# Kernel optimization log

Hardware: AMD Instinct MI355X
Metric: run time of the kernel (lower is better)

The kernel has to match this reference:

```python
import jax, jax.numpy as jnp
import numpy as np

D = 128          # lattice edge (Z = Y = X = 128)
S = 8            # state_size
H = 16           # hidden_size
IN = 7 * S       # own state + 6 neighbor states = 56


def setup_inputs() -> dict:
    key = jax.random.key(0)
    k0, k1, k2 = jax.random.split(key, 3)
    N = D * D * D
    states = jax.random.normal(k0, (N, S), dtype=jnp.float32)
    W1 = jax.random.normal(k1, (IN, H), dtype=jnp.float32) * (1.0 / np.sqrt(IN))
    b1 = jnp.zeros((H,), dtype=jnp.float32)
    W2 = jax.random.normal(k2, (H, S), dtype=jnp.float32) * (1.0 / np.sqrt(H))
    b2 = jnp.zeros((S,), dtype=jnp.float32)
    return {"states": states, "W1": W1, "b1": b1, "W2": W2, "b2": b2}


def reference(states, W1, b1, W2, b2):
    # linear index = z*(X*Y) + y*X + x  ->  grid layout (Z, Y, X, S)
    g = states.reshape(D, D, D, S)
    # 6-neighbor gather with periodic boundary (NEIGHBOR_DIRECTIONS order:
    # (-1,0,0),(1,0,0),(0,-1,0),(0,1,0),(0,0,-1),(0,0,1)); x->axis2, y->axis1, z->axis0.
    # roll(+1) along an axis fetches the neighbor in the -1 direction.
    nbrs = [
        jnp.roll(g,  1, axis=2),  # x-1
        jnp.roll(g, -1, axis=2),  # x+1
        jnp.roll(g,  1, axis=1),  # y-1
        jnp.roll(g, -1, axis=1),  # y+1
        jnp.roll(g,  1, axis=0),  # z-1
        jnp.roll(g, -1, axis=0),  # z+1
    ]
    inp = jnp.concatenate([g] + nbrs, axis=-1)          # (Z, Y, X, 56)
    h = jnp.tanh(jnp.einsum('zyxi,ih->zyxh', inp, W1) + b1)
    out = jnp.einsum('zyxh,hs->zyxs', h, W2) + b2        # (Z, Y, X, 8)
    return out.reshape(-1, S)
```

## Files before the change

kernel.cpp:

```cpp
#include <hip/hip_runtime.h>

#define DIM 128
#define SLOT_STRIDE 2096

typedef __attribute__((ext_vector_type(8))) short bf16x8;
typedef __attribute__((ext_vector_type(4))) float f32x4;
typedef __attribute__((ext_vector_type(4))) unsigned int u32x4;

static __device__ __forceinline__ unsigned short f2bf_rne(float f) {
    union { float f; unsigned int i; } c; c.f = f;
    unsigned int u = c.i;
    return (unsigned short)((u + 0x7fffu + ((u >> 16) & 1u)) >> 16);
}
static __device__ __forceinline__ unsigned int fbits(float f) {
    union { float f; unsigned int i; } c; c.f = f; return c.i;
}
static __device__ __forceinline__ unsigned int pack_bf16_rne(float lo, float hi) {
    unsigned int ul = fbits(lo), uh = fbits(hi);
    unsigned int tl = ul + 0x7fffu + ((ul >> 16) & 1u);
    unsigned int th = uh + 0x7fffu + ((uh >> 16) & 1u);
    return __builtin_amdgcn_perm(th, tl, 0x07060302u);
}

struct Frags {
    bf16x8 w1h0, w1h1, w2h;
    f32x4 b1v, b2v;
};

static __device__ __forceinline__ void build_frags(
    const float* W1, const float* b1, const float* W2, const float* b2,
    int col, int quad, Frags& F)
{
#pragma unroll
    for (int j = 0; j < 8; ++j) {
        int k0 = quad * 8 + j;
        F.w1h0[j] = (short)f2bf_rne(W1[k0 * 16 + col]);
        int k1 = 32 + quad * 8 + j;
        F.w1h1[j] = (short)f2bf_rne((k1 < 56) ? W1[k1 * 16 + col] : 0.0f);
        float w2 = (j < 4 && col < 8) ? W2[(quad * 4 + j) * 8 + col] : 0.0f;
        F.w2h[j] = (short)f2bf_rne(w2);
    }
#pragma unroll
    for (int r = 0; r < 4; ++r) {
        F.b1v[r] = b1[quad * 4 + r];
        F.b2v[r] = (quad < 2) ? b2[quad * 4 + r] : 0.0f;
    }
}

__global__ __launch_bounds__(64) void setup_kernel(
    const float* __restrict__ W1, const float* __restrict__ b1,
    const float* __restrict__ W2, const float* __restrict__ b2,
    u32x4* __restrict__ ws)
{
    const int lane = threadIdx.x;
    Frags F;
    build_frags(W1, b1, W2, b2, lane & 15, lane >> 4, F);
    union { bf16x8 v; u32x4 u; } c;
    c.v = F.w1h0; ws[0 * 64 + lane] = c.u;
    c.v = F.w1h1; ws[1 * 64 + lane] = c.u;
    c.v = F.w2h;  ws[2 * 64 + lane] = c.u;
    union { f32x4 v; u32x4 u; } b;
    b.v = F.b1v; ws[3 * 64 + lane] = b.u;
    b.v = F.b2v; ws[4 * 64 + lane] = b.u;
}

template<bool USE_WS>
__global__ __launch_bounds__(256, 5) void lattice_kernel(
    const float* __restrict__ states,
    const float* __restrict__ W1, const float* __restrict__ b1,
    const float* __restrict__ W2, const float* __restrict__ b2,
    float* __restrict__ out, const u32x4* __restrict__ ws)
{
    __shared__ __align__(16) unsigned char lds[15 * SLOT_STRIDE];

    const int tid  = threadIdx.x;
    const int lane = tid & 63;
    const int w    = __builtin_amdgcn_readfirstlane(tid >> 6);
    const int col  = lane & 15;
    const int quad = lane >> 4;

    Frags F;
    if (USE_WS) {
        union { u32x4 u; bf16x8 v; } c;
        c.u = ws[0 * 64 + lane]; F.w1h0 = c.v;
        c.u = ws[1 * 64 + lane]; F.w1h1 = c.v;
        c.u = ws[2 * 64 + lane]; F.w2h  = c.v;
        union { u32x4 u; f32x4 v; } b;
        b.u = ws[3 * 64 + lane]; F.b1v = b.v;
        b.u = ws[4 * 64 + lane]; F.b2v = b.v;
    } else {
        build_frags(W1, b1, W2, b2, col, quad, F);
    }

    const int bI   = blockIdx.x;
    const int slab = bI & 7;
    const int inr  = bI >> 3;
    const int z    = slab * 16 + (inr >> 5);
    const int y0   = (inr & 31) << 2;

    f32x4 ga[7], gb[7];
#pragma unroll
    for (int i = 0; i < 7; ++i) {
        const int tk   = w * 7 + i;
        const int slot = (tk < 20) ? (tk >> 1) : 11 + ((tk - 20) >> 1);
        const int half = tk & 1;
        int yr, zr;
        if (slot < 6)       { yr = (y0 - 1 + slot) & 127; zr = z; }
        else if (slot < 10) { yr = y0 + (slot - 6);       zr = (z - 1) & 127; }
        else                { yr = y0 + (slot - 11);      zr = (z + 1) & 127; }
        const float* g = states + ((size_t)(zr * 16384 + yr * 128 + half * 64) << 3);
        ga[i] = *(const f32x4*)(g + (lane << 3));
        gb[i] = *(const f32x4*)(g + (lane << 3) + 4);
    }
#pragma unroll
    for (int i = 0; i < 7; ++i) {
        const int tk   = w * 7 + i;
        const int slot = (tk < 20) ? (tk >> 1) : 11 + ((tk - 20) >> 1);
        const int half = tk & 1;
        u32x4 p;
        p[0] = __builtin_amdgcn_perm(fbits(ga[i][1]), fbits(ga[i][0]), 0x07060302u);
        p[1] = __builtin_amdgcn_perm(fbits(ga[i][3]), fbits(ga[i][2]), 0x07060302u);
        p[2] = __builtin_amdgcn_perm(fbits(gb[i][1]), fbits(gb[i][0]), 0x07060302u);
        p[3] = __builtin_amdgcn_perm(fbits(gb[i][3]), fbits(gb[i][2]), 0x07060302u);
        const int base = slot * SLOT_STRIDE;
        *(u32x4*)(lds + base + ((half * 64 + lane + 1) << 4)) = p;
        if (half == 0 && lane == 0)  *(u32x4*)(lds + base + 2064) = p;
        if (half == 1 && lane == 63) *(u32x4*)(lds + base) = p;
    }
    __syncthreads();

    const int dxA   = (quad == 1) ? -1 : (quad == 2) ? 1 : 0;
    const int slotA = (quad == 3) ? w : w + 1;
    const int slotB = (quad == 1) ? 6 + w : (quad == 2) ? 11 + w : w + 2;
    const unsigned char* pA = lds + slotA * SLOT_STRIDE + ((col + dxA + 1) << 4);
    const unsigned char* pB = lds + slotB * SLOT_STRIDE + ((col + 1) << 4);

    float* pO = out + (size_t)((z * 16384 + (y0 + w) * 128 + col) * 8 + quad * 4);

#pragma unroll
    for (int i = 0; i < 8; ++i) {
        bf16x8 s0f = *(const bf16x8*)(pA + (i << 8));
        bf16x8 s1f = *(const bf16x8*)(pB + (i << 8));

        f32x4 acc = F.b1v;
        acc = __builtin_amdgcn_mfma_f32_16x16x32_bf16(F.w1h0, s0f, acc, 0, 0, 0);
        acc = __builtin_amdgcn_mfma_f32_16x16x32_bf16(F.w1h1, s1f, acc, 0, 0, 0);

        float h0t, h1t, h2t, h3t;
        {
            float e;
            e = __expf(2.0f * acc[0]); h0t = 1.0f - 2.0f * __builtin_amdgcn_rcpf(e + 1.0f);
            e = __expf(2.0f * acc[1]); h1t = 1.0f - 2.0f * __builtin_amdgcn_rcpf(e + 1.0f);
            e = __expf(2.0f * acc[2]); h2t = 1.0f - 2.0f * __builtin_amdgcn_rcpf(e + 1.0f);
            e = __expf(2.0f * acc[3]); h3t = 1.0f - 2.0f * __builtin_amdgcn_rcpf(e + 1.0f);
        }
        union { bf16x8 v; unsigned int u[4]; } hf;
        hf.u[0] = pack_bf16_rne(h0t, h1t);
        hf.u[1] = pack_bf16_rne(h2t, h3t);
        hf.u[2] = 0u;
        hf.u[3] = 0u;

        f32x4 acc2 = F.b2v;
        acc2 = __builtin_amdgcn_mfma_f32_16x16x32_bf16(F.w2h, hf.v, acc2, 0, 0, 0);

        if (quad < 2) {
            __builtin_nontemporal_store(acc2, (f32x4*)(pO + (i << 7)));
        }
    }
}

extern "C" void kernel_launch(void* const* d_in, const int* in_sizes, int n_in,
                              void* d_out, int out_size, void* d_ws, size_t ws_size,
                              hipStream_t stream) {
    const float* states = (const float*)d_in[0];
    const float* W1     = (const float*)d_in[1];
    const float* b1     = (const float*)d_in[2];
    const float* W2     = (const float*)d_in[3];
    const float* b2     = (const float*)d_in[4];
    float* out          = (float*)d_out;

    const bool use_ws = ws_size >= (size_t)(5 * 64 * 16);
    if (use_ws) {
        hipLaunchKernelGGL(setup_kernel, dim3(1), dim3(64), 0, stream,
                           W1, b1, W2, b2, (u32x4*)d_ws);
        hipLaunchKernelGGL((lattice_kernel<true>), dim3(4096), dim3(256), 0, stream,
                           states, W1, b1, W2, b2, out, (const u32x4*)d_ws);
    } else {
        hipLaunchKernelGGL((lattice_kernel<false>), dim3(4096), dim3(256), 0, stream,
                           states, W1, b1, W2, b2, out, (const u32x4*)d_ws);
    }
}
```

Before: 122.1 us.

## March each block through four z-planes with a rotating three-plane LDS ring

Each block now processes four consecutive z-planes instead of one, keeping the previous, current and next planes (6 y-rows each) in a three-slot LDS ring. It prefetches plane z+2 into registers while computing the current plane. This removes the redundant re-reading of z-neighbor rows across blocks, cutting global traffic from about 14 rows per output plane to about 6. In exchange the grid shrinks to 1024 blocks, occupancy is lowered to 4 blocks per SM, and extra barriers are added per plane, which reduces parallelism and may expose latency.

```diff
diff --git a/kernel.cpp b/kernel.cpp
--- a/kernel.cpp
+++ b/kernel.cpp
@@ -2,6 +2,7 @@
 
 #define DIM 128
 #define SLOT_STRIDE 2096
+#define PLANE_STRIDE (6 * SLOT_STRIDE)
 
 typedef __attribute__((ext_vector_type(8))) short bf16x8;
 typedef __attribute__((ext_vector_type(4))) float f32x4;
@@ -65,13 +66,13 @@
 }
 
 template<bool USE_WS>
-__global__ __launch_bounds__(256, 5) void lattice_kernel(
+__global__ __launch_bounds__(256, 4) void lattice_kernel(
     const float* __restrict__ states,
     const float* __restrict__ W1, const float* __restrict__ b1,
     const float* __restrict__ W2, const float* __restrict__ b2,
     float* __restrict__ out, const u32x4* __restrict__ ws)
 {
-    __shared__ __align__(16) unsigned char lds[15 * SLOT_STRIDE];
+    __shared__ __align__(16) unsigned char lds[3 * PLANE_STRIDE];
 
     const int tid  = threadIdx.x;
     const int lane = tid & 63;
@@ -95,76 +96,102 @@
     const int bI   = blockIdx.x;
     const int slab = bI & 7;
     const int inr  = bI >> 3;
-    const int z    = slab * 16 + (inr >> 5);
+    const int z0   = ((slab << 2) + (inr >> 5)) << 2;
     const int y0   = (inr & 31) << 2;
 
-    f32x4 ga[7], gb[7];
-#pragma unroll
-    for (int i = 0; i < 7; ++i) {
-        const int tk   = w * 7 + i;
-        const int slot = (tk < 20) ? (tk >> 1) : 11 + ((tk - 20) >> 1);
-        const int half = tk & 1;
-        int yr, zr;
-        if (slot < 6)       { yr = (y0 - 1 + slot) & 127; zr = z; }
-        else if (slot < 10) { yr = y0 + (slot - 6);       zr = (z - 1) & 127; }
-        else                { yr = y0 + (slot - 11);      zr = (z + 1) & 127; }
-        const float* g = states + ((size_t)(zr * 16384 + yr * 128 + half * 64) << 3);
-        ga[i] = *(const f32x4*)(g + (lane << 3));
-        gb[i] = *(const f32x4*)(g + (lane << 3) + 4);
-    }
-#pragma unroll
-    for (int i = 0; i < 7; ++i) {
-        const int tk   = w * 7 + i;
-        const int slot = (tk < 20) ? (tk >> 1) : 11 + ((tk - 20) >> 1);
-        const int half = tk & 1;
-        u32x4 p;
-        p[0] = __builtin_amdgcn_perm(fbits(ga[i][1]), fbits(ga[i][0]), 0x07060302u);
-        p[1] = __builtin_amdgcn_perm(fbits(ga[i][3]), fbits(ga[i][2]), 0x07060302u);
-        p[2] = __builtin_amdgcn_perm(fbits(gb[i][1]), fbits(gb[i][0]), 0x07060302u);
-        p[3] = __builtin_amdgcn_perm(fbits(gb[i][3]), fbits(gb[i][2]), 0x07060302u);
-        const int base = slot * SLOT_STRIDE;
-        *(u32x4*)(lds + base + ((half * 64 + lane + 1) << 4)) = p;
-        if (half == 0 && lane == 0)  *(u32x4*)(lds + base + 2064) = p;
-        if (half == 1 && lane == 63) *(u32x4*)(lds + base) = p;
-    }
+    auto issue_plane = [&](int zp, f32x4* a, f32x4* b) {
+#pragma unroll
+        for (int i = 0; i < 3; ++i) {
+            const int tk   = w * 3 + i;
+            const int r    = tk >> 1;
+            const int half = tk & 1;
+            const int yr   = (y0 - 1 + r) & 127;
+            const float* g = states +
+                ((size_t)((((unsigned)(zp & 127)) << 14) + (yr << 7) + (half << 6)) << 3);
+            a[i] = *(const f32x4*)(g + (lane << 3));
+            b[i] = *(const f32x4*)(g + (lane << 3) + 4);
+        }
+    };
+    auto write_plane = [&](int buf, const f32x4* a, const f32x4* b) {
+#pragma unroll
+        for (int i = 0; i < 3; ++i) {
+            const int tk   = w * 3 + i;
+            const int r    = tk >> 1;
+            const int half = tk & 1;
+            u32x4 p;
+            p[0] = __builtin_amdgcn_perm(fbits(a[i][1]), fbits(a[i][0]), 0x07060302u);
+            p[1] = __builtin_amdgcn_perm(fbits(a[i][3]), fbits(a[i][2]), 0x07060302u);
+            p[2] = __builtin_amdgcn_perm(fbits(b[i][1]), fbits(b[i][0]), 0x07060302u);
+            p[3] = __builtin_amdgcn_perm(fbits(b[i][3]), fbits(b[i][2]), 0x07060302u);
+            unsigned char* base = lds + buf * PLANE_STRIDE + r * SLOT_STRIDE;
+            *(u32x4*)(base + ((half * 64 + lane + 1) << 4)) = p;
+            if (half == 0 && lane == 0)  *(u32x4*)(base + 2064) = p;
+            if (half == 1 && lane == 63) *(u32x4*)(base) = p;
+        }
+    };
+
+    f32x4 gA[3], gB[3], hA[3], hB[3];
+    issue_plane(z0 - 1, gA, gB);
+    issue_plane(z0,     hA, hB);
+    write_plane(0, gA, gB);
+    issue_plane(z0 + 1, gA, gB);
+    write_plane(1, hA, hB);
+    write_plane(2, gA, gB);
     __syncthreads();
 
-    const int dxA   = (quad == 1) ? -1 : (quad == 2) ? 1 : 0;
-    const int slotA = (quad == 3) ? w : w + 1;
-    const int slotB = (quad == 1) ? 6 + w : (quad == 2) ? 11 + w : w + 2;
-    const unsigned char* pA = lds + slotA * SLOT_STRIDE + ((col + dxA + 1) << 4);
-    const unsigned char* pB = lds + slotB * SLOT_STRIDE + ((col + 1) << 4);
-
-    float* pO = out + (size_t)((z * 16384 + (y0 + w) * 128 + col) * 8 + quad * 4);
-
-#pragma unroll
-    for (int i = 0; i < 8; ++i) {
-        bf16x8 s0f = *(const bf16x8*)(pA + (i << 8));
-        bf16x8 s1f = *(const bf16x8*)(pB + (i << 8));
-
-        f32x4 acc = F.b1v;
-        acc = __builtin_amdgcn_mfma_f32_16x16x32_bf16(F.w1h0, s0f, acc, 0, 0, 0);
-        acc = __builtin_amdgcn_mfma_f32_16x16x32_bf16(F.w1h1, s1f, acc, 0, 0, 0);
-
-        float h0t, h1t, h2t, h3t;
-        {
-            float e;
-            e = __expf(2.0f * acc[0]); h0t = 1.0f - 2.0f * __builtin_amdgcn_rcpf(e + 1.0f);
-            e = __expf(2.0f * acc[1]); h1t = 1.0f - 2.0f * __builtin_amdgcn_rcpf(e + 1.0f);
-            e = __expf(2.0f * acc[2]); h2t = 1.0f - 2.0f * __builtin_amdgcn_rcpf(e + 1.0f);
-            e = __expf(2.0f * acc[3]); h3t = 1.0f - 2.0f * __builtin_amdgcn_rcpf(e + 1.0f);
-        }
-        union { bf16x8 v; unsigned int u[4]; } hf;
-        hf.u[0] = pack_bf16_rne(h0t, h1t);
-        hf.u[1] = pack_bf16_rne(h2t, h3t);
-        hf.u[2] = 0u;
-        hf.u[3] = 0u;
-
-        f32x4 acc2 = F.b2v;
-        acc2 = __builtin_amdgcn_mfma_f32_16x16x32_bf16(F.w2h, hf.v, acc2, 0, 0, 0);
-
-        if (quad < 2) {
-            __builtin_nontemporal_store(acc2, (f32x4*)(pO + (i << 7)));
+    const int dxA  = (quad == 1) ? -1 : (quad == 2) ? 1 : 0;
+    const int rA   = (quad == 3) ? w : w + 1;
+    const int rB   = (quad == 0) ? w + 2 : w + 1;
+    const int offA = rA * SLOT_STRIDE + ((col + dxA + 1) << 4);
+    const int offB = rB * SLOT_STRIDE + ((col + 1) << 4);
+
+#pragma unroll
+    for (int s = 0; s < 4; ++s) {
+        const int zc = z0 + s;
+        if (s < 3) issue_plane(zc + 2, gA, gB);
+
+        const int bufZm = s % 3, bufZ = (s + 1) % 3, bufZp = (s + 2) % 3;
+        const unsigned char* pA = lds + bufZ * PLANE_STRIDE + offA;
+        const int bB = (quad == 1) ? bufZm : (quad == 2) ? bufZp : bufZ;
+        const unsigned char* pB = lds + bB * PLANE_STRIDE + offB;
+
+        float* pO = out + (size_t)(((zc << 14) + ((y0 + w) << 7) + col) * 8 + quad * 4);
+
+#pragma unroll
+        for (int i = 0; i < 8; ++i) {
+            bf16x8 s0f = *(const bf16x8*)(pA + (i << 8));
+            bf16x8 s1f = *(const bf16x8*)(pB + (i << 8));
+
+            f32x4 acc = F.b1v;
+            acc = __builtin_amdgcn_mfma_f32_16x16x32_bf16(F.w1h0, s0f, acc, 0, 0, 0);
+            acc = __builtin_amdgcn_mfma_f32_16x16x32_bf16(F.w1h1, s1f, acc, 0, 0, 0);
+
+            float h0t, h1t, h2t, h3t;
+            {
+                float e;
+                e = __expf(2.0f * acc[0]); h0t = 1.0f - 2.0f * __builtin_amdgcn_rcpf(e + 1.0f);
+                e = __expf(2.0f * acc[1]); h1t = 1.0f - 2.0f * __builtin_amdgcn_rcpf(e + 1.0f);
+                e = __expf(2.0f * acc[2]); h2t = 1.0f - 2.0f * __builtin_amdgcn_rcpf(e + 1.0f);
+                e = __expf(2.0f * acc[3]); h3t = 1.0f - 2.0f * __builtin_amdgcn_rcpf(e + 1.0f);
+            }
+            union { bf16x8 v; unsigned int u[4]; } hf;
+            hf.u[0] = pack_bf16_rne(h0t, h1t);
+            hf.u[1] = pack_bf16_rne(h2t, h3t);
+            hf.u[2] = 0u;
+            hf.u[3] = 0u;
+
+            f32x4 acc2 = F.b2v;
+            acc2 = __builtin_amdgcn_mfma_f32_16x16x32_bf16(F.w2h, hf.v, acc2, 0, 0, 0);
+
+            if (quad < 2) {
+                __builtin_nontemporal_store(acc2, (f32x4*)(pO + (i << 7)));
+            }
+        }
+
+        __syncthreads();
+        if (s < 3) {
+            write_plane(bufZm, gA, gB);
+            __syncthreads();
         }
     }
 }
@@ -183,10 +210,10 @@
     if (use_ws) {
         hipLaunchKernelGGL(setup_kernel, dim3(1), dim3(64), 0, stream,
                            W1, b1, W2, b2, (u32x4*)d_ws);
-        hipLaunchKernelGGL((lattice_kernel<true>), dim3(4096), dim3(256), 0, stream,
+        hipLaunchKernelGGL((lattice_kernel<true>), dim3(1024), dim3(256), 0, stream,
                            states, W1, b1, W2, b2, out, (const u32x4*)d_ws);
     } else {
-        hipLaunchKernelGGL((lattice_kernel<false>), dim3(4096), dim3(256), 0, stream,
+        hipLaunchKernelGGL((lattice_kernel<false>), dim3(1024), dim3(256), 0, stream,
                            states, W1, b1, W2, b2, out, (const u32x4*)d_ws);
     }
 }
```

New measurement: 122.5 us. Within noise of the previous version (+0.4%).

## Enlarge block tile to 4z×4y rows to reuse staged neighbor rows

Applied to the files above, without the earlier changes.

Each block now covers 4 z-planes by 4 y-rows with 512 threads, staging 32 rows (halo included) in LDS instead of 15 rows for a single z-plane. The goal is to cut redundant global reads of halo rows, from 15 per 4 output rows to 32 per 16. Periodic x wrap now uses masked indexing instead of padded halo slots. The barrier becomes an LDS-only wait, and stores are batched after all MFMAs. The trade-off is fewer, larger blocks with more registers held per thread.

```diff
diff --git a/kernel.cpp b/kernel.cpp
--- a/kernel.cpp
+++ b/kernel.cpp
@@ -1,7 +1,7 @@
 #include <hip/hip_runtime.h>
 
-#define DIM 128
-#define SLOT_STRIDE 2096
+#define SLOT 2048
+#define NSLOT 32
 
 typedef __attribute__((ext_vector_type(8))) short bf16x8;
 typedef __attribute__((ext_vector_type(4))) float f32x4;
@@ -20,6 +20,12 @@
     unsigned int tl = ul + 0x7fffu + ((ul >> 16) & 1u);
     unsigned int th = uh + 0x7fffu + ((uh >> 16) & 1u);
     return __builtin_amdgcn_perm(th, tl, 0x07060302u);
+}
+
+static __device__ __forceinline__ void barrier_lds_only() {
+    asm volatile("s_waitcnt lgkmcnt(0)" ::: "memory");
+    __builtin_amdgcn_s_barrier();
+    __builtin_amdgcn_sched_barrier(0);
 }
 
 struct Frags {
@@ -65,13 +71,13 @@
 }
 
 template<bool USE_WS>
-__global__ __launch_bounds__(256, 5) void lattice_kernel(
+__global__ __launch_bounds__(512, 4) void lattice_kernel(
     const float* __restrict__ states,
     const float* __restrict__ W1, const float* __restrict__ b1,
     const float* __restrict__ W2, const float* __restrict__ b2,
     float* __restrict__ out, const u32x4* __restrict__ ws)
 {
-    __shared__ __align__(16) unsigned char lds[15 * SLOT_STRIDE];
+    __shared__ __align__(16) unsigned char lds[NSLOT * SLOT];
 
     const int tid  = threadIdx.x;
     const int lane = tid & 63;
@@ -95,76 +101,90 @@
     const int bI   = blockIdx.x;
     const int slab = bI & 7;
     const int inr  = bI >> 3;
-    const int z    = slab * 16 + (inr >> 5);
+    const int z0   = slab * 16 + ((inr >> 5) << 2);
     const int y0   = (inr & 31) << 2;
 
-    f32x4 ga[7], gb[7];
-#pragma unroll
-    for (int i = 0; i < 7; ++i) {
-        const int tk   = w * 7 + i;
-        const int slot = (tk < 20) ? (tk >> 1) : 11 + ((tk - 20) >> 1);
-        const int half = tk & 1;
-        int yr, zr;
-        if (slot < 6)       { yr = (y0 - 1 + slot) & 127; zr = z; }
-        else if (slot < 10) { yr = y0 + (slot - 6);       zr = (z - 1) & 127; }
-        else                { yr = y0 + (slot - 11);      zr = (z + 1) & 127; }
-        const float* g = states + ((size_t)(zr * 16384 + yr * 128 + half * 64) << 3);
+    f32x4 ga[8], gb[8];
+#pragma unroll
+    for (int i = 0; i < 8; ++i) {
+        const int tk = w * 8 + i;
+        const int s  = tk >> 1, half = tk & 1;
+        int zr, yr;
+        if (s < 4)       { zr = z0 - 1; yr = y0 + s; }
+        else if (s < 28) { const int t = s - 4, p = t / 6, r = t - 6 * p;
+                           zr = z0 + p; yr = y0 - 1 + r; }
+        else             { zr = z0 + 4; yr = y0 + (s - 28); }
+        zr &= 127; yr &= 127;
+        const float* g = states + ((size_t)((zr << 14) + (yr << 7) + (half << 6)) << 3);
         ga[i] = *(const f32x4*)(g + (lane << 3));
         gb[i] = *(const f32x4*)(g + (lane << 3) + 4);
     }
 #pragma unroll
-    for (int i = 0; i < 7; ++i) {
-        const int tk   = w * 7 + i;
-        const int slot = (tk < 20) ? (tk >> 1) : 11 + ((tk - 20) >> 1);
-        const int half = tk & 1;
+    for (int i = 0; i < 8; ++i) {
+        const int tk = w * 8 + i;
+        const int s  = tk >> 1, half = tk & 1;
         u32x4 p;
         p[0] = __builtin_amdgcn_perm(fbits(ga[i][1]), fbits(ga[i][0]), 0x07060302u);
         p[1] = __builtin_amdgcn_perm(fbits(ga[i][3]), fbits(ga[i][2]), 0x07060302u);
         p[2] = __builtin_amdgcn_perm(fbits(gb[i][1]), fbits(gb[i][0]), 0x07060302u);
         p[3] = __builtin_amdgcn_perm(fbits(gb[i][3]), fbits(gb[i][2]), 0x07060302u);
-        const int base = slot * SLOT_STRIDE;
-        *(u32x4*)(lds + base + ((half * 64 + lane + 1) << 4)) = p;
-        if (half == 0 && lane == 0)  *(u32x4*)(lds + base + 2064) = p;
-        if (half == 1 && lane == 63) *(u32x4*)(lds + base) = p;
-    }
-    __syncthreads();
-
-    const int dxA   = (quad == 1) ? -1 : (quad == 2) ? 1 : 0;
-    const int slotA = (quad == 3) ? w : w + 1;
-    const int slotB = (quad == 1) ? 6 + w : (quad == 2) ? 11 + w : w + 2;
-    const unsigned char* pA = lds + slotA * SLOT_STRIDE + ((col + dxA + 1) << 4);
-    const unsigned char* pB = lds + slotB * SLOT_STRIDE + ((col + 1) << 4);
-
-    float* pO = out + (size_t)((z * 16384 + (y0 + w) * 128 + col) * 8 + quad * 4);
-
-#pragma unroll
-    for (int i = 0; i < 8; ++i) {
-        bf16x8 s0f = *(const bf16x8*)(pA + (i << 8));
-        bf16x8 s1f = *(const bf16x8*)(pB + (i << 8));
-
-        f32x4 acc = F.b1v;
-        acc = __builtin_amdgcn_mfma_f32_16x16x32_bf16(F.w1h0, s0f, acc, 0, 0, 0);
-        acc = __builtin_amdgcn_mfma_f32_16x16x32_bf16(F.w1h1, s1f, acc, 0, 0, 0);
-
-        float h0t, h1t, h2t, h3t;
-        {
-            float e;
-            e = __expf(2.0f * acc[0]); h0t = 1.0f - 2.0f * __builtin_amdgcn_rcpf(e + 1.0f);
-            e = __expf(2.0f * acc[1]); h1t = 1.0f - 2.0f * __builtin_amdgcn_rcpf(e + 1.0f);
-            e = __expf(2.0f * acc[2]); h2t = 1.0f - 2.0f * __builtin_amdgcn_rcpf(e + 1.0f);
-            e = __expf(2.0f * acc[3]); h3t = 1.0f - 2.0f * __builtin_amdgcn_rcpf(e + 1.0f);
+        *(u32x4*)(lds + s * SLOT + ((half * 64 + lane) << 4)) = p;
+    }
+    barrier_lds_only();
+
+    const int zs  = w >> 1;
+    const int Bz  = 4 + 6 * zs;
+    const int zc  = z0 + zs;
+    const int dxA = (quad == 1) ? -1 : (quad == 2) ? 1 : 0;
+    const int cA  = col + dxA;
+
+#pragma unroll
+    for (int j = 0; j < 2; ++j) {
+        const int rc    = 2 * (w & 1) + j;
+        const int slotA = (quad == 3) ? (Bz + rc) : (Bz + rc + 1);
+        int slotB;
+        if (quad == 0)      slotB = Bz + rc + 2;
+        else if (quad == 1) slotB = (zs == 0) ? rc : (Bz - 6 + rc + 1);
+        else if (quad == 2) slotB = (zs == 3) ? (28 + rc) : (Bz + 6 + rc + 1);
+        else                slotB = Bz + rc + 1;
+        const unsigned char* pA = lds + slotA * SLOT;
+        const unsigned char* pB = lds + slotB * SLOT + (col << 4);
+        float* pO = out + (size_t)(((zc << 14) + ((y0 + rc) << 7) + col) * 8 + quad * 4);
+
+        f32x4 accs[8];
+#pragma unroll
+        for (int i = 0; i < 8; ++i) {
+            const int cellA = (i * 16 + cA) & 127;
+            bf16x8 s0f = *(const bf16x8*)(pA + (cellA << 4));
+            bf16x8 s1f = *(const bf16x8*)(pB + (i << 8));
+
+            f32x4 acc = F.b1v;
+            acc = __builtin_amdgcn_mfma_f32_16x16x32_bf16(F.w1h0, s0f, acc, 0, 0, 0);
+            acc = __builtin_amdgcn_mfma_f32_16x16x32_bf16(F.w1h1, s1f, acc, 0, 0, 0);
+
+            float h0t, h1t, h2t, h3t;
+            {
+                float e;
+                e = __expf(2.0f * acc[0]); h0t = 1.0f - 2.0f * __builtin_amdgcn_rcpf(e + 1.0f);
+                e = __expf(2.0f * acc[1]); h1t = 1.0f - 2.0f * __builtin_amdgcn_rcpf(e + 1.0f);
+                e = __expf(2.0f * acc[2]); h2t = 1.0f - 2.0f * __builtin_amdgcn_rcpf(e + 1.0f);
+                e = __expf(2.0f * acc[3]); h3t = 1.0f - 2.0f * __builtin_amdgcn_rcpf(e + 1.0f);
+            }
+            union { bf16x8 v; unsigned int u[4]; } hf;
+            hf.u[0] = pack_bf16_rne(h0t, h1t);
+            hf.u[1] = pack_bf16_rne(h2t, h3t);
+            hf.u[2] = 0u;
+            hf.u[3] = 0u;
+
+            f32x4 a2 = F.b2v;
+            a2 = __builtin_amdgcn_mfma_f32_16x16x32_bf16(F.w2h, hf.v, a2, 0, 0, 0);
+            accs[i] = a2;
         }
-        union { bf16x8 v; unsigned int u[4]; } hf;
-        hf.u[0] = pack_bf16_rne(h0t, h1t);
-        hf.u[1] = pack_bf16_rne(h2t, h3t);
-        hf.u[2] = 0u;
-        hf.u[3] = 0u;
-
-        f32x4 acc2 = F.b2v;
-        acc2 = __builtin_amdgcn_mfma_f32_16x16x32_bf16(F.w2h, hf.v, acc2, 0, 0, 0);
-
         if (quad < 2) {
-            __builtin_nontemporal_store(acc2, (f32x4*)(pO + (i << 7)));
+#pragma unroll
+            for (int i = 0; i < 8; ++i) {
+                __builtin_nontemporal_store(accs[i], (f32x4*)(pO + (i << 7)));
+            }
         }
     }
 }
@@ -183,10 +203,10 @@
     if (use_ws) {
         hipLaunchKernelGGL(setup_kernel, dim3(1), dim3(64), 0, stream,
                            W1, b1, W2, b2, (u32x4*)d_ws);
-        hipLaunchKernelGGL((lattice_kernel<true>), dim3(4096), dim3(256), 0, stream,
+        hipLaunchKernelGGL((lattice_kernel<true>), dim3(1024), dim3(512), 0, stream,
                            states, W1, b1, W2, b2, out, (const u32x4*)d_ws);
     } else {
-        hipLaunchKernelGGL((lattice_kernel<false>), dim3(4096), dim3(256), 0, stream,
+        hipLaunchKernelGGL((lattice_kernel<false>), dim3(1024), dim3(512), 0, stream,
                            states, W1, b1, W2, b2, out, (const u32x4*)d_ws);
     }
 }
```

New measurement: 122.6 us. Within noise of the previous version (+0.4%).

## Drop LDS staging; load neighbor rows directly from global per MFMA fragment

Applied to the files above, without the earlier changes.

Removes the shared-memory halo staging and barrier. Each lane now loads its own and neighbor cells straight from global memory and converts them to bf16 in registers. Each block covers two rows per wave, so the grid is halved and the occupancy hint is lowered to 4. The aim is to avoid the LDS write/read round trip and the sync, at the cost of redundant global/L2 reads of shared neighbor rows. Outputs are buffered and written after each row's compute.

```diff
diff --git a/kernel.cpp b/kernel.cpp
--- a/kernel.cpp
+++ b/kernel.cpp
@@ -1,7 +1,4 @@
 #include <hip/hip_runtime.h>
-
-#define DIM 128
-#define SLOT_STRIDE 2096
 
 typedef __attribute__((ext_vector_type(8))) short bf16x8;
 typedef __attribute__((ext_vector_type(4))) float f32x4;
@@ -65,14 +62,12 @@
 }
 
 template<bool USE_WS>
-__global__ __launch_bounds__(256, 5) void lattice_kernel(
+__global__ __launch_bounds__(256, 4) void lattice_kernel(
     const float* __restrict__ states,
     const float* __restrict__ W1, const float* __restrict__ b1,
     const float* __restrict__ W2, const float* __restrict__ b2,
     float* __restrict__ out, const u32x4* __restrict__ ws)
 {
-    __shared__ __align__(16) unsigned char lds[15 * SLOT_STRIDE];
-
     const int tid  = threadIdx.x;
     const int lane = tid & 63;
     const int w    = __builtin_amdgcn_readfirstlane(tid >> 6);
@@ -95,78 +90,79 @@
     const int bI   = blockIdx.x;
     const int slab = bI & 7;
     const int inr  = bI >> 3;
-    const int z    = slab * 16 + (inr >> 5);
-    const int y0   = (inr & 31) << 2;
+    const int z    = slab * 16 + (inr >> 4);
+    const int yo   = (inr & 15) << 3;
 
-    f32x4 ga[7], gb[7];
+    const int dxA = (quad == 1) ? -1 : (quad == 2) ? 1 : 0;
+    const int xA0 = col + dxA;
+
+    auto do_row = [&](int y) {
+        const int ym = (y + 127) & 127, yp = (y + 1) & 127;
+        const int zm = (z + 127) & 127, zp = (z + 1) & 127;
+        const float* b_own = states + ((size_t)((z  << 14) + (y  << 7)) << 3);
+        const float* b_ym  = states + ((size_t)((z  << 14) + (ym << 7)) << 3);
+        const float* b_yp  = states + ((size_t)((z  << 14) + (yp << 7)) << 3);
+        const float* b_zm  = states + ((size_t)((zm << 14) + (y  << 7)) << 3);
+        const float* b_zp  = states + ((size_t)((zp << 14) + (y  << 7)) << 3);
+        const float* bA = (quad == 3) ? b_ym : b_own;
+        const float* bB = (quad == 0) ? b_yp : (quad == 1) ? b_zm
+                        : (quad == 2) ? b_zp : b_own;
+        float* pO = out + (size_t)(((z << 14) + (y << 7) + col) * 8 + quad * 4);
+
+        f32x4 accs[8];
 #pragma unroll
-    for (int i = 0; i < 7; ++i) {
-        const int tk   = w * 7 + i;
-        const int slot = (tk < 20) ? (tk >> 1) : 11 + ((tk - 20) >> 1);
-        const int half = tk & 1;
-        int yr, zr;
-        if (slot < 6)       { yr = (y0 - 1 + slot) & 127; zr = z; }
-        else if (slot < 10) { yr = y0 + (slot - 6);       zr = (z - 1) & 127; }
-        else                { yr = y0 + (slot - 11);      zr = (z + 1) & 127; }
-        const float* g = states + ((size_t)(zr * 16384 + yr * 128 + half * 64) << 3);
-        ga[i] = *(const f32x4*)(g + (lane << 3));
-        gb[i] = *(const f32x4*)(g + (lane << 3) + 4);
-    }
+        for (int i = 0; i < 8; ++i) {
+            const int xA = (xA0 + (i << 4)) & 127;
+            const int xB = col + (i << 4);
+            const float* pa = bA + ((size_t)xA << 3);
+            const float* pb = bB + ((size_t)xB << 3);
+            f32x4 a0 = *(const f32x4*)(pa);
+            f32x4 a1 = *(const f32x4*)(pa + 4);
+            f32x4 c0 = *(const f32x4*)(pb);
+            f32x4 c1 = *(const f32x4*)(pb + 4);
+
+            union { bf16x8 v; unsigned int u[4]; } s0, s1;
+            s0.u[0] = pack_bf16_rne(a0[0], a0[1]);
+            s0.u[1] = pack_bf16_rne(a0[2], a0[3]);
+            s0.u[2] = pack_bf16_rne(a1[0], a1[1]);
+            s0.u[3] = pack_bf16_rne(a1[2], a1[3]);
+            s1.u[0] = pack_bf16_rne(c0[0], c0[1]);
+            s1.u[1] = pack_bf16_rne(c0[2], c0[3]);
+            s1.u[2] = pack_bf16_rne(c1[0], c1[1]);
+            s1.u[3] = pack_bf16_rne(c1[2], c1[3]);
+
+            f32x4 acc = F.b1v;
+            acc = __builtin_amdgcn_mfma_f32_16x16x32_bf16(F.w1h0, s0.v, acc, 0, 0, 0);
+            acc = __builtin_amdgcn_mfma_f32_16x16x32_bf16(F.w1h1, s1.v, acc, 0, 0, 0);
+
+            float h0t, h1t, h2t, h3t;
+            {
+                float e;
+                e = __expf(2.0f * acc[0]); h0t = 1.0f - 2.0f * __builtin_amdgcn_rcpf(e + 1.0f);
+                e = __expf(2.0f * acc[1]); h1t = 1.0f - 2.0f * __builtin_amdgcn_rcpf(e + 1.0f);
+                e = __expf(2.0f * acc[2]); h2t = 1.0f - 2.0f * __builtin_amdgcn_rcpf(e + 1.0f);
+                e = __expf(2.0f * acc[3]); h3t = 1.0f - 2.0f * __builtin_amdgcn_rcpf(e + 1.0f);
+            }
+            union { bf16x8 v; unsigned int u[4]; } hf;
+            hf.u[0] = pack_bf16_rne(h0t, h1t);
+            hf.u[1] = pack_bf16_rne(h2t, h3t);
+            hf.u[2] = 0u;
+            hf.u[3] = 0u;
+
+            f32x4 a2 = F.b2v;
+            a2 = __builtin_amdgcn_mfma_f32_16x16x32_bf16(F.w2h, hf.v, a2, 0, 0, 0);
+            accs[i] = a2;
+        }
+        if (quad < 2) {
 #pragma unroll
-    for (int i = 0; i < 7; ++i) {
-        const int tk   = w * 7 + i;
-        const int slot = (tk < 20) ? (tk >> 1) : 11 + ((tk - 20) >> 1);
-        const int half = tk & 1;
-        u32x4 p;
-        p[0] = __builtin_amdgcn_perm(fbits(ga[i][1]), fbits(ga[i][0]), 0x07060302u);
-        p[1] = __builtin_amdgcn_perm(fbits(ga[i][3]), fbits(ga[i][2]), 0x07060302u);
-        p[2] = __builtin_amdgcn_perm(fbits(gb[i][1]), fbits(gb[i][0]), 0x07060302u);
-        p[3] = __builtin_amdgcn_perm(fbits(gb[i][3]), fbits(gb[i][2]), 0x07060302u);
-        const int base = slot * SLOT_STRIDE;
-        *(u32x4*)(lds + base + ((half * 64 + lane + 1) << 4)) = p;
-        if (half == 0 && lane == 0)  *(u32x4*)(lds + base + 2064) = p;
-        if (half == 1 && lane == 63) *(u32x4*)(lds + base) = p;
-    }
-    __syncthreads();
+            for (int i = 0; i < 8; ++i) {
+                __builtin_nontemporal_store(accs[i], (f32x4*)(pO + (i << 7)));
+            }
+        }
+    };
 
-    const int dxA   = (quad == 1) ? -1 : (quad == 2) ? 1 : 0;
-    const int slotA = (quad == 3) ? w : w + 1;
-    const int slotB = (quad == 1) ? 6 + w : (quad == 2) ? 11 + w : w + 2;
-    const unsigned char* pA = lds + slotA * SLOT_STRIDE + ((col + dxA + 1) << 4);
-    const unsigned char* pB = lds + slotB * SLOT_STRIDE + ((col + 1) << 4);
-
-    float* pO = out + (size_t)((z * 16384 + (y0 + w) * 128 + col) * 8 + quad * 4);
-
-#pragma unroll
-    for (int i = 0; i < 8; ++i) {
-        bf16x8 s0f = *(const bf16x8*)(pA + (i << 8));
-        bf16x8 s1f = *(const bf16x8*)(pB + (i << 8));
-
-        f32x4 acc = F.b1v;
-        acc = __builtin_amdgcn_mfma_f32_16x16x32_bf16(F.w1h0, s0f, acc, 0, 0, 0);
-        acc = __builtin_amdgcn_mfma_f32_16x16x32_bf16(F.w1h1, s1f, acc, 0, 0, 0);
-
-        float h0t, h1t, h2t, h3t;
-        {
-            float e;
-            e = __expf(2.0f * acc[0]); h0t = 1.0f - 2.0f * __builtin_amdgcn_rcpf(e + 1.0f);
-            e = __expf(2.0f * acc[1]); h1t = 1.0f - 2.0f * __builtin_amdgcn_rcpf(e + 1.0f);
-            e = __expf(2.0f * acc[2]); h2t = 1.0f - 2.0f * __builtin_amdgcn_rcpf(e + 1.0f);
-            e = __expf(2.0f * acc[3]); h3t = 1.0f - 2.0f * __builtin_amdgcn_rcpf(e + 1.0f);
-        }
-        union { bf16x8 v; unsigned int u[4]; } hf;
-        hf.u[0] = pack_bf16_rne(h0t, h1t);
-        hf.u[1] = pack_bf16_rne(h2t, h3t);
-        hf.u[2] = 0u;
-        hf.u[3] = 0u;
-
-        f32x4 acc2 = F.b2v;
-        acc2 = __builtin_amdgcn_mfma_f32_16x16x32_bf16(F.w2h, hf.v, acc2, 0, 0, 0);
-
-        if (quad < 2) {
-            __builtin_nontemporal_store(acc2, (f32x4*)(pO + (i << 7)));
-        }
-    }
+    do_row(yo + w);
+    do_row(yo + w + 4);
 }
 
 extern "C" void kernel_launch(void* const* d_in, const int* in_sizes, int n_in,
@@ -183,10 +179,10 @@
     if (use_ws) {
         hipLaunchKernelGGL(setup_kernel, dim3(1), dim3(64), 0, stream,
                            W1, b1, W2, b2, (u32x4*)d_ws);
-        hipLaunchKernelGGL((lattice_kernel<true>), dim3(4096), dim3(256), 0, stream,
+        hipLaunchKernelGGL((lattice_kernel<true>), dim3(2048), dim3(256), 0, stream,
                            states, W1, b1, W2, b2, out, (const u32x4*)d_ws);
     } else {
-        hipLaunchKernelGGL((lattice_kernel<false>), dim3(4096), dim3(256), 0, stream,
+        hipLaunchKernelGGL((lattice_kernel<false>), dim3(2048), dim3(256), 0, stream,
                            states, W1, b1, W2, b2, out, (const u32x4*)d_ws);
     }
 }
```

Result: slower. 131.2 us (+7.5%).
